# Kernel optimization log

Hardware: AMD Instinct MI355X
Metric: run time of the kernel (lower is better)

The kernel has to match this reference:

```python
import jax, jax.numpy as jnp
import numpy as np

N_NODES = 100000
N_EDGES = 1600000
D = 128
HID = 256  # min(2*D, 256)
D_OUT = 128
BN_EPS = 1e-5


def setup_inputs() -> dict:
    key = jax.random.key(0)
    ks = jax.random.split(key, 16)
    s = 0.05
    inp = {
        "x": jax.random.normal(ks[0], (N_NODES, D), dtype=jnp.float32),
        "edges": jax.random.randint(ks[1], (2, N_EDGES), 0, N_NODES, dtype=jnp.int32),
        # affine_before_rnn: Linear(D, D)
        "W_aff": jax.random.normal(ks[2], (D, D), dtype=jnp.float32) * s,
        "b_aff": jnp.zeros((D,), dtype=jnp.float32),
        # GRUCell(D, D)
        "W_ih": jax.random.normal(ks[3], (3 * D, D), dtype=jnp.float32) * s,
        "b_ih": jnp.zeros((3 * D,), dtype=jnp.float32),
        "W_hh": jax.random.normal(ks[4], (3 * D, D), dtype=jnp.float32) * s,
        "b_hh": jnp.zeros((3 * D,), dtype=jnp.float32),
        # merge_layer: Linear(2*D, D)
        "W_merge": jax.random.normal(ks[5], (D, 2 * D), dtype=jnp.float32) * s,
        "b_merge": jnp.zeros((D,), dtype=jnp.float32),
        # learnable self-connection weight
        "eps": jnp.asarray(1.0, dtype=jnp.float32),
        # backbone: Linear(D, HID) -> relu -> Linear(HID, D_OUT) -> relu -> BatchNorm1d
        "W1": jax.random.normal(ks[6], (HID, D), dtype=jnp.float32) * s,
        "b1": jnp.zeros((HID,), dtype=jnp.float32),
        "W2": jax.random.normal(ks[7], (D_OUT, HID), dtype=jnp.float32) * s,
        "b2": jnp.zeros((D_OUT,), dtype=jnp.float32),
        "gamma": jnp.ones((D_OUT,), dtype=jnp.float32),
        "beta": jnp.zeros((D_OUT,), dtype=jnp.float32),
    }
    return inp


def reference(x, edges, W_aff, b_aff, W_ih, b_ih, W_hh, b_hh,
              W_merge, b_merge, eps, W1, b1, W2, b2, gamma, beta):
    src, dst = edges[0], edges[1]
    n = x.shape[0]

    # ---- aggregation 1: 'sum' -> scatter-sum of neighbor features ----
    agg_sum = jax.ops.segment_sum(x[src], dst, num_segments=n)  # (N, D)

    # ---- aggregation 2: 'rnn-max' -> affine, scatter-max, GRUCell ----
    xi = x @ W_aff.T + b_aff
    agg_max = jax.ops.segment_max(xi[src], dst, num_segments=n)  # (N, D)
    agg_max = jnp.where(jnp.isfinite(agg_max), agg_max, 0.0)  # empty segments -> 0

    # GRUCell: input = aggregated neighbors, hidden = original node features
    gi = agg_max @ W_ih.T + b_ih  # (N, 3D)
    gh = x @ W_hh.T + b_hh        # (N, 3D)
    ir, iz, inn = jnp.split(gi, 3, axis=1)
    hr, hz, hn = jnp.split(gh, 3, axis=1)
    r = jax.nn.sigmoid(ir + hr)
    z = jax.nn.sigmoid(iz + hz)
    ncand = jnp.tanh(inn + r * hn)
    rnn_out = (1.0 - z) * ncand + z * x  # (N, D)

    # ---- merge ('cat') ----
    h = jnp.concatenate([agg_sum, rnn_out], axis=1) @ W_merge.T + b_merge  # (N, D)

    # ---- learnable self-connection ----
    h = h + eps * x

    # ---- backbone: dense -> relu -> dense -> relu -> batchnorm1d (train mode) ----
    h = jax.nn.relu(h @ W1.T + b1)
    h = jax.nn.relu(h @ W2.T + b2)
    mean = jnp.mean(h, axis=0)
    var = jnp.mean(jnp.square(h - mean), axis=0)  # biased batch variance
    out = gamma * (h - mean) * jax.lax.rsqrt(var + BN_EPS) + beta
    return out
```

## Files before the change

### kernel.cpp

```cpp
#include <hip/hip_runtime.h>
#include <hip/hip_bf16.h>
#include <math.h>

using bf16 = __hip_bfloat16;
typedef __attribute__((ext_vector_type(8))) short bf16x8;
typedef __attribute__((ext_vector_type(4))) float f32x4;

__device__ __forceinline__ float b2f(unsigned short u) {
  return __uint_as_float(((unsigned)u) << 16);
}
__device__ __forceinline__ unsigned short f2b(float f) {
  bf16 h = __float2bfloat16(f);
  return *reinterpret_cast<unsigned short*>(&h);
}
__device__ __forceinline__ ushort4 f2b4(float4 v) {
  return make_ushort4(f2b(v.x), f2b(v.y), f2b(v.z), f2b(v.w));
}

__global__ __launch_bounds__(256) void mgemm_k(
    const unsigned short* __restrict__ A, int lda, const float* __restrict__ W,
    const float* __restrict__ bias, unsigned short* __restrict__ Cb, int ldc,
    int N, int M, int K) {
  constexpr int LDA = 72;
  __shared__ unsigned short As[128 * LDA];
  __shared__ unsigned short Ws[128 * LDA];

  const int tid = threadIdx.x;
  const int lane = tid & 63;
  const int wave = tid >> 6;
  const int row0 = blockIdx.y * 128;
  const int m0 = blockIdx.x * 128;
  const int rowhalf = (wave & 1) * 64;
  const int colhalf = (wave >> 1) * 64;
  const int l15 = lane & 15;
  const int quad = lane >> 4;

  f32x4 acc[4][4] = {};

  for (int kc = 0; kc < K; kc += 64) {
#pragma unroll
    for (int i = 0; i < 4; i++) {
      int idx = tid + i * 256;
      int r = idx >> 3;
      int k8 = (idx & 7) * 8;
      int row = row0 + r;
      ushort4 u0 = make_ushort4(0, 0, 0, 0), u1 = u0;
      if (row < N) {
        const unsigned short* s = A + (size_t)row * lda + kc + k8;
        u0 = *(const ushort4*)s;
        u1 = *(const ushort4*)(s + 4);
      }
      *(ushort4*)&As[r * LDA + k8] = u0;
      *(ushort4*)&As[r * LDA + k8 + 4] = u1;
    }
#pragma unroll
    for (int i = 0; i < 8; i++) {
      int idx = tid + i * 256;
      int r = idx >> 4;
      int k4 = idx & 15;
      float4 v = *(const float4*)(W + (size_t)(m0 + r) * K + kc + k4 * 4);
      *(ushort4*)&Ws[r * LDA + k4 * 4] = f2b4(v);
    }
    __syncthreads();
#pragma unroll
    for (int ks = 0; ks < 2; ks++) {
      const int ko = ks * 32 + quad * 8;
      bf16x8 af[4], wf[4];
#pragma unroll
      for (int ri = 0; ri < 4; ri++)
        af[ri] = *(const bf16x8*)&As[(rowhalf + ri * 16 + l15) * LDA + ko];
#pragma unroll
      for (int ci = 0; ci < 4; ci++)
        wf[ci] = *(const bf16x8*)&Ws[(colhalf + ci * 16 + l15) * LDA + ko];
#pragma unroll
      for (int ri = 0; ri < 4; ri++)
#pragma unroll
        for (int ci = 0; ci < 4; ci++)
          acc[ri][ci] = __builtin_amdgcn_mfma_f32_16x16x32_bf16(
              af[ri], wf[ci], acc[ri][ci], 0, 0, 0);
    }
    __syncthreads();
  }
#pragma unroll
  for (int ci = 0; ci < 4; ci++) {
    const int col = m0 + colhalf + ci * 16 + l15;
    const float bv = bias[col];
#pragma unroll
    for (int ri = 0; ri < 4; ri++) {
      const int rbase = row0 + rowhalf + ri * 16 + quad * 4;
#pragma unroll
      for (int r = 0; r < 4; r++) {
        int row = rbase + r;
        if (row >= N) continue;
        Cb[(size_t)row * ldc + col] = f2b(acc[ri][ci][r] + bv);
      }
    }
  }
}

__global__ __launch_bounds__(256) void grubb_k(
    const unsigned short* __restrict__ aggm,
    const unsigned short* __restrict__ xcat,
    const unsigned short* __restrict__ aggs,
    const unsigned short* __restrict__ Wbig,
    const float* __restrict__ bias_big,
    const unsigned short* __restrict__ Wmb, const float* __restrict__ bm,
    const unsigned short* __restrict__ W1b, const float* __restrict__ b1,
    const unsigned short* __restrict__ W2b, const float* __restrict__ b2,
    const float* __restrict__ epsp, float* __restrict__ out,
    float* __restrict__ stats, int N) {
  constexpr int LDA = 264;
  constexpr int LDH = 136;
  __shared__ unsigned short As[32 * LDA];
  __shared__ unsigned short Acat[32 * LDA];
  __shared__ unsigned short Hp[32 * LDH];
  __shared__ float sbn[128], qbn[128];
  unsigned short* Hd = As;

  const int tid = threadIdx.x;
  const int lane = tid & 63;
  const int wave = tid >> 6;
  const int l15 = lane & 15;
  const int quad = lane >> 4;
  const int row0 = blockIdx.x * 32;
  if (tid < 128) {
    sbn[tid] = 0.f;
    qbn[tid] = 0.f;
  }
  const float ep = epsp[0];

  {
    int r = tid >> 3;
    int k32 = (tid & 7) * 32;
    int row = row0 + r;
    uint4 u[4] = {};
    uint4 v[2] = {};
    if (row < N) {
      const unsigned short* s = (k32 < 128)
                                    ? aggm + (size_t)row * 128 + k32
                                    : xcat + (size_t)row * 256 + (k32 - 128);
#pragma unroll
      for (int i = 0; i < 4; i++) u[i] = *(const uint4*)(s + i * 8);
      const unsigned short* s2 = aggs + (size_t)row * 128 + (tid & 7) * 16;
      v[0] = *(const uint4*)s2;
      v[1] = *(const uint4*)(s2 + 8);
    }
#pragma unroll
    for (int i = 0; i < 4; i++) *(uint4*)&As[r * LDA + k32 + i * 8] = u[i];
    int k16 = (tid & 7) * 16;
    *(uint4*)&Acat[r * LDA + k16] = v[0];
    *(uint4*)&Acat[r * LDA + k16 + 8] = v[1];
  }
  __syncthreads();

  {
    f32x4 acc[2][8] = {};
#pragma unroll
    for (int ks = 0; ks < 8; ks++) {
      const int ko = ks * 32 + quad * 8;
      bf16x8 af0 = *(const bf16x8*)&As[l15 * LDA + ko];
      bf16x8 af1 = *(const bf16x8*)&As[(16 + l15) * LDA + ko];
#pragma unroll
      for (int ci = 0; ci < 8; ci++) {
        int m = wave * 128 + ci * 16 + l15;
        bf16x8 wf = *(const bf16x8*)&Wbig[(size_t)m * 256 + ko];
        acc[0][ci] = __builtin_amdgcn_mfma_f32_16x16x32_bf16(af0, wf,
                                                             acc[0][ci], 0, 0, 0);
        acc[1][ci] = __builtin_amdgcn_mfma_f32_16x16x32_bf16(af1, wf,
                                                             acc[1][ci], 0, 0, 0);
      }
    }
#pragma unroll
    for (int fi = 0; fi < 2; fi++) {
      const int f = wave * 32 + fi * 16 + l15;
      const float br = bias_big[f];
      const float bz = bias_big[128 + f];
      const float bi = bias_big[256 + f];
      const float bh = bias_big[384 + f];
#pragma unroll
      for (int ri = 0; ri < 2; ri++) {
#pragma unroll
        for (int r = 0; r < 4; r++) {
          int rl = ri * 16 + quad * 4 + r;
          float rg = 1.f / (1.f + __expf(-(acc[ri][4 * fi + 0][r] + br)));
          float zg = 1.f / (1.f + __expf(-(acc[ri][4 * fi + 1][r] + bz)));
          float a =
              acc[ri][4 * fi + 2][r] + bi + rg * (acc[ri][4 * fi + 3][r] + bh);
          float t = 1.f - 2.f / (__expf(2.f * fabsf(a)) + 1.f);
          float nc = copysignf(t, a);
          float xv = b2f(As[rl * LDA + 128 + f]);
          Acat[rl * LDA + 128 + f] = f2b((1.f - zg) * nc + zg * xv);
        }
      }
    }
  }
  __syncthreads();

  {
    f32x4 accm[2][2] = {};
#pragma unroll
    for (int ks = 0; ks < 8; ks++) {
      const int ko = ks * 32 + quad * 8;
      bf16x8 af[2];
#pragma unroll
      for (int ri = 0; ri < 2; ri++)
        af[ri] = *(const bf16x8*)&Acat[(ri * 16 + l15) * LDA + ko];
#pragma unroll
      for (int ci = 0; ci < 2; ci++) {
        bf16x8 wf =
            *(const bf16x8*)&Wmb[(size_t)(wave * 32 + ci * 16 + l15) * 256 + ko];
#pragma unroll
        for (int ri = 0; ri < 2; ri++)
          accm[ri][ci] = __builtin_amdgcn_mfma_f32_16x16x32_bf16(
              af[ri], wf, accm[ri][ci], 0, 0, 0);
      }
    }
#pragma unroll
    for (int ci = 0; ci < 2; ci++) {
      int c = wave * 32 + ci * 16 + l15;
      float bv = bm[c];
#pragma unroll
      for (int ri = 0; ri < 2; ri++) {
#pragma unroll
        for (int r = 0; r < 4; r++) {
          int rl = ri * 16 + quad * 4 + r;
          float v = accm[ri][ci][r] + bv + ep * b2f(As[rl * LDA + 128 + c]);
          Hp[rl * LDH + c] = f2b(v);
        }
      }
    }
  }
  __syncthreads();

  f32x4 acc3[2][2] = {};
#pragma unroll
  for (int hh = 0; hh < 2; hh++) {
    f32x4 acc2[2][2] = {};
#pragma unroll
    for (int ks = 0; ks < 4; ks++) {
      const int ko = ks * 32 + quad * 8;
      bf16x8 af[2];
#pragma unroll
      for (int ri = 0; ri < 2; ri++)
        af[ri] = *(const bf16x8*)&Hp[(ri * 16 + l15) * LDH + ko];
#pragma unroll
      for (int ci = 0; ci < 2; ci++) {
        bf16x8 wf = *(const bf16x8*)&W1b[(size_t)(hh * 128 + wave * 32 +
                                                  ci * 16 + l15) *
                                             128 +
                                         ko];
#pragma unroll
        for (int ri = 0; ri < 2; ri++)
          acc2[ri][ci] = __builtin_amdgcn_mfma_f32_16x16x32_bf16(
              af[ri], wf, acc2[ri][ci], 0, 0, 0);
      }
    }
    __syncthreads();
#pragma unroll
    for (int ci = 0; ci < 2; ci++) {
      int c = wave * 32 + ci * 16 + l15;
      float bv = b1[hh * 128 + c];
#pragma unroll
      for (int ri = 0; ri < 2; ri++) {
#pragma unroll
        for (int r = 0; r < 4; r++) {
          int rl = ri * 16 + quad * 4 + r;
          Hd[rl * LDH + c] = f2b(fmaxf(acc2[ri][ci][r] + bv, 0.f));
        }
      }
    }
    __syncthreads();
#pragma unroll
    for (int ks = 0; ks < 4; ks++) {
      const int ko = ks * 32 + quad * 8;
      bf16x8 af[2];
#pragma unroll
      for (int ri = 0; ri < 2; ri++)
        af[ri] = *(const bf16x8*)&Hd[(ri * 16 + l15) * LDH + ko];
#pragma unroll
      for (int ci = 0; ci < 2; ci++) {
        bf16x8 wf = *(const bf16x8*)&W2b[(size_t)(wave * 32 + ci * 16 + l15) *
                                             256 +
                                         hh * 128 + ko];
#pragma unroll
        for (int ri = 0; ri < 2; ri++)
          acc3[ri][ci] = __builtin_amdgcn_mfma_f32_16x16x32_bf16(
              af[ri], wf, acc3[ri][ci], 0, 0, 0);
      }
    }
  }
#pragma unroll
  for (int ci = 0; ci < 2; ci++) {
    int c = wave * 32 + ci * 16 + l15;
    float bv = b2[c];
    float s = 0.f, q = 0.f;
#pragma unroll
    for (int ri = 0; ri < 2; ri++) {
#pragma unroll
      for (int r = 0; r < 4; r++) {
        int rl = ri * 16 + quad * 4 + r;
        int row = row0 + rl;
        if (row >= N) continue;
        float v = fmaxf(acc3[ri][ci][r] + bv, 0.f);
        out[(size_t)row * 128 + c] = v;
        s += v;
        q += v * v;
      }
    }
    atomicAdd(&sbn[c], s);
    atomicAdd(&qbn[c], q);
  }
  __syncthreads();
  if (tid < 128) {
    atomicAdd(&stats[tid], sbn[tid]);
    atomicAdd(&stats[128 + tid], qbn[tid]);
  }
}

__global__ __launch_bounds__(256) void prep_k(
    const float* __restrict__ W_ih, const float* __restrict__ b_ih,
    const float* __restrict__ W_hh, const float* __restrict__ b_hh,
    const float* __restrict__ Wm, const float* __restrict__ W1,
    const float* __restrict__ W2, unsigned short* __restrict__ Wbig,
    unsigned short* __restrict__ Wmb, unsigned short* __restrict__ W1b,
    unsigned short* __restrict__ W2b, float* __restrict__ bias_big,
    float* __restrict__ stats, int* __restrict__ deg, int N) {
  int idx = blockIdx.x * 256 + threadIdx.x;
  if (idx < N) deg[idx] = 0;
  if (idx < 32768) {
    int mp = idx >> 6;
    int k4 = (idx & 63) * 4;
    int w = mp >> 7, ci = (mp >> 4) & 7, l15 = mp & 15;
    int g = ci & 3, fi = ci >> 2;
    int f = w * 32 + fi * 16 + l15;
    const float* src = nullptr;
    int koff = 0;
    if (g <= 1) {
      int m = g * 128 + f;
      if (k4 < 128) { src = W_ih + (size_t)m * 128; koff = k4; }
      else          { src = W_hh + (size_t)m * 128; koff = k4 - 128; }
    } else if (g == 2) {
      if (k4 < 128) { src = W_ih + (size_t)(256 + f) * 128; koff = k4; }
    } else {
      if (k4 >= 128) { src = W_hh + (size_t)(256 + f) * 128; koff = k4 - 128; }
    }
    ushort4 o = make_ushort4(0, 0, 0, 0);
    if (src) o = f2b4(*(const float4*)(src + koff));
    *(ushort4*)&Wbig[(size_t)mp * 256 + k4] = o;
  }
  if (idx < 8192) {
    int m = idx >> 6;
    int k4 = (idx & 63) * 4;
    *(ushort4*)&Wmb[(size_t)m * 256 + k4] =
        f2b4(*(const float4*)(Wm + (size_t)m * 256 + k4));
    *(ushort4*)&W2b[(size_t)m * 256 + k4] =
        f2b4(*(const float4*)(W2 + (size_t)m * 256 + k4));
    int m2 = idx >> 5;
    int k42 = (idx & 31) * 4;
    *(ushort4*)&W1b[(size_t)m2 * 128 + k42] =
        f2b4(*(const float4*)(W1 + (size_t)m2 * 128 + k42));
  }
  if (blockIdx.x == 0) {
    int t = threadIdx.x;
    stats[t] = 0.f;
#pragma unroll
    for (int h = 0; h < 2; h++) {
      int mm = t + h * 256;
      float b;
      if (mm < 256) b = b_ih[mm] + b_hh[mm];
      else if (mm < 384) b = b_ih[mm];
      else b = b_hh[mm - 128];
      bias_big[mm] = b;
    }
  }
}

__global__ __launch_bounds__(256) void cvthist_k(
    const int* __restrict__ edges, int* __restrict__ deg, int E,
    const float* __restrict__ x, unsigned short* __restrict__ xcat,
    int ngroups, int eblk) {
  if ((int)blockIdx.x < eblk) {
    int e = blockIdx.x * 256 + threadIdx.x;
    if (e < E) atomicAdd(&deg[edges[(size_t)E + e]], 1);
  } else {
    int g = (blockIdx.x - eblk) * 256 + threadIdx.x;
    if (g >= ngroups) return;
    int n = g >> 5;
    int j = (g & 31) * 4;
    float4 v = *(const float4*)&x[(size_t)n * 128 + j];
    *(ushort4*)&xcat[(size_t)n * 256 + j] = f2b4(v);
  }
}

__global__ __launch_bounds__(256) void scan1_k(const int* __restrict__ deg,
                                               int* __restrict__ off,
                                               int* __restrict__ bsums, int N) {
  __shared__ int s[256];
  int t = threadIdx.x;
  int i = blockIdx.x * 256 + t;
  int v = (i < N) ? deg[i] : 0;
  s[t] = v;
  __syncthreads();
#pragma unroll
  for (int d = 1; d < 256; d <<= 1) {
    int u = (t >= d) ? s[t - d] : 0;
    __syncthreads();
    s[t] += u;
    __syncthreads();
  }
  if (i < N) off[i] = s[t] - v;
  if (t == 255) bsums[blockIdx.x] = s[255];
}

__global__ __launch_bounds__(512) void scan2_k(int* __restrict__ bsums,
                                               int nb) {
  __shared__ int s[512];
  int t = threadIdx.x;
  int v = (t < nb) ? bsums[t] : 0;
  s[t] = v;
  __syncthreads();
#pragma unroll
  for (int d = 1; d < 512; d <<= 1) {
    int u = (t >= d) ? s[t - d] : 0;
    __syncthreads();
    s[t] += u;
    __syncthreads();
  }
  if (t < nb) bsums[t] = s[t] - v;
}

__global__ __launch_bounds__(256) void scan3_k(int* __restrict__ off,
                                               const int* __restrict__ bsums,
                                               int* __restrict__ binoff,
                                               int* __restrict__ bincur,
                                               int N, int E, int NB) {
  int i = blockIdx.x * 256 + threadIdx.x;
  if (i < N) {
    int o = off[i] + bsums[blockIdx.x];
    off[i] = o;
    if ((i & 511) == 0) {
      binoff[i >> 9] = o;
      bincur[i >> 9] = o;
    }
  }
  if (i == 0) {
    off[N] = E;
    binoff[NB] = E;
  }
}

__global__ __launch_bounds__(256) void edgepart_k(const int* __restrict__ edges,
                                                  int* __restrict__ bincur,
                                                  int* __restrict__ part,
                                                  int E, int NB) {
  __shared__ int cnt[256];
  const int tid = threadIdx.x;
  if (tid < NB) cnt[tid] = 0;
  __syncthreads();
  int sv[16], dv[16];
  const int e0 = blockIdx.x * 4096;
#pragma unroll
  for (int i = 0; i < 16; i++) {
    int e = e0 + i * 256 + tid;
    int s = 0, d = -1;
    if (e < E) {
      s = edges[e];
      d = edges[(size_t)E + e];
    }
    sv[i] = s;
    dv[i] = d;
    if (d >= 0) atomicAdd(&cnt[d >> 9], 1);
  }
  __syncthreads();
  if (tid < NB) {
    int c = cnt[tid];
    int base = c ? atomicAdd(&bincur[tid], c) : 0;
    cnt[tid] = base;
  }
  __syncthreads();
#pragma unroll
  for (int i = 0; i < 16; i++) {
    int d = dv[i];
    if (d < 0) continue;
    int p = atomicAdd(&cnt[d >> 9], 1);
    part[p] = (sv[i] << 9) | (d & 511);
  }
}

__global__ __launch_bounds__(1024) void fill2_k(const int* __restrict__ off,
                                                const int* __restrict__ binoff,
                                                const int* __restrict__ part,
                                                int* __restrict__ bucket,
                                                int N) {
  __shared__ int scur[512];
  const int b = blockIdx.x;
  const int n0 = b << 9;
  const int tid = threadIdx.x;
  if (tid < 512) {
    int node = n0 + tid;
    scur[tid] = (node < N) ? off[node] : 0;
  }
  __syncthreads();
  const int j0 = binoff[b];
  const int j1 = binoff[b + 1];
  for (int j = j0 + tid; j < j1; j += 1024) {
    int p = part[j];
    int pos = atomicAdd(&scur[p & 511], 1);
    bucket[pos] = p >> 9;
  }
}

__global__ __launch_bounds__(256) void gather_k(
    const int* __restrict__ off, const int* __restrict__ bucket,
    const unsigned short* __restrict__ xcat, unsigned short* __restrict__ aggm,
    unsigned short* __restrict__ aggs, int N) {
  int node = blockIdx.x * 4 + (threadIdx.x >> 6);
  if (node >= N) return;
  const int lane = threadIdx.x & 63;
  const int half = lane >> 5;
  const int f = (lane & 31) * 4;
  const int j0 = off[node], jend = off[node + 1];
  float s0 = 0.f, s1 = 0.f, s2 = 0.f, s3 = 0.f;
  float m0 = -INFINITY, m1 = -INFINITY, m2 = -INFINITY, m3 = -INFINITY;
  int jj = j0 + half;
  int p0 = (jj < jend) ? bucket[jj] : 0;
  int p1 = (jj + 2 < jend) ? bucket[jj + 2] : 0;
  for (; jj < jend; jj += 2) {
    int src = p0;
    p0 = p1;
    p1 = (jj + 4 < jend) ? bucket[jj + 4] : 0;
    ushort4 a = *(const ushort4*)(xcat + (size_t)src * 256 + f);
    ushort4 b = *(const ushort4*)(xcat + (size_t)src * 256 + 128 + f);
    s0 += b2f(a.x);
    s1 += b2f(a.y);
    s2 += b2f(a.z);
    s3 += b2f(a.w);
    m0 = fmaxf(m0, b2f(b.x));
    m1 = fmaxf(m1, b2f(b.y));
    m2 = fmaxf(m2, b2f(b.z));
    m3 = fmaxf(m3, b2f(b.w));
  }
  s0 += __shfl_xor(s0, 32);
  s1 += __shfl_xor(s1, 32);
  s2 += __shfl_xor(s2, 32);
  s3 += __shfl_xor(s3, 32);
  m0 = fmaxf(m0, __shfl_xor(m0, 32));
  m1 = fmaxf(m1, __shfl_xor(m1, 32));
  m2 = fmaxf(m2, __shfl_xor(m2, 32));
  m3 = fmaxf(m3, __shfl_xor(m3, 32));
  if (half == 0) {
    bool nz = jend > j0;
    ushort4 mv = nz ? make_ushort4(f2b(m0), f2b(m1), f2b(m2), f2b(m3))
                    : make_ushort4(0, 0, 0, 0);
    *(ushort4*)&aggm[(size_t)node * 128 + f] = mv;
    *(ushort4*)&aggs[(size_t)node * 128 + f] =
        make_ushort4(f2b(s0), f2b(s1), f2b(s2), f2b(s3));
  }
}

__global__ __launch_bounds__(256) void bn_apply_k(
    float* __restrict__ out, const float* __restrict__ stats,
    const float* __restrict__ gamma, const float* __restrict__ beta,
    float invn, int nd4) {
  int g = blockIdx.x * 256 + threadIdx.x;
  if (g >= nd4) return;
  int d = (g & 31) * 4;
  float4 v = ((float4*)out)[g];
  float o[4] = {v.x, v.y, v.z, v.w};
#pragma unroll
  for (int i = 0; i < 4; i++) {
    float mean = stats[d + i] * invn;
    float var = fmaxf(stats[128 + d + i] * invn - mean * mean, 0.f);
    float sc = gamma[d + i] * rsqrtf(var + 1e-5f);
    o[i] = (o[i] - mean) * sc + beta[d + i];
  }
  ((float4*)out)[g] = make_float4(o[0], o[1], o[2], o[3]);
}

extern "C" void kernel_launch(void* const* d_in, const int* in_sizes, int n_in,
                              void* d_out, int out_size, void* d_ws,
                              size_t ws_size, hipStream_t stream) {
  (void)n_in;
  (void)out_size;
  (void)ws_size;
  const float* x = (const float*)d_in[0];
  const int* edges = (const int*)d_in[1];
  const float* W_aff = (const float*)d_in[2];
  const float* b_aff = (const float*)d_in[3];
  const float* W_ih = (const float*)d_in[4];
  const float* b_ih = (const float*)d_in[5];
  const float* W_hh = (const float*)d_in[6];
  const float* b_hh = (const float*)d_in[7];
  const float* W_merge = (const float*)d_in[8];
  const float* b_merge = (const float*)d_in[9];
  const float* epsp = (const float*)d_in[10];
  const float* W1 = (const float*)d_in[11];
  const float* b1 = (const float*)d_in[12];
  const float* W2 = (const float*)d_in[13];
  const float* b2 = (const float*)d_in[14];
  const float* gamma = (const float*)d_in[15];
  const float* beta = (const float*)d_in[16];

  const int N = in_sizes[0] / 128;
  const int E = in_sizes[1] / 2;
  const size_t nd = (size_t)N * 128;
  const int NB = (N + 511) >> 9;

  char* base = (char*)d_ws;
  unsigned short* xcat = (unsigned short*)base;
  unsigned short* aggs = (unsigned short*)(base + (size_t)N * 512);
  unsigned short* aggm = (unsigned short*)(base + (size_t)N * 1024);
  unsigned short* Wbig = (unsigned short*)(base + (size_t)N * 1280);
  unsigned short* Wmb = Wbig + 512 * 256;
  unsigned short* W1b = Wmb + 128 * 256;
  unsigned short* W2b = W1b + 256 * 128;
  float* bias_big = (float*)(W2b + 128 * 256);
  float* stats = bias_big + 512;
  int* deg = (int*)(stats + 512);
  int* off = deg + N;
  int* binoff = off + N + 1;
  int* bincur = binoff + NB + 1;
  int* bucket = bincur + NB;
  int* bsums = bucket + E;
  float* out = (float*)d_out;
  int* part = (int*)d_out;

  const int ny = (N + 127) / 128;
  const int nblk = (N + 255) / 256;
  const int eblk = (E + 255) / 256;
  const int cvtblk = (int)((nd / 4 + 255) / 256);
  const int pgrid = nblk > 128 ? nblk : 128;
  dim3 blk(256);

  prep_k<<<pgrid, blk, 0, stream>>>(W_ih, b_ih, W_hh, b_hh, W_merge, W1, W2,
                                    Wbig, Wmb, W1b, W2b, bias_big, stats, deg,
                                    N);
  cvthist_k<<<eblk + cvtblk, blk, 0, stream>>>(edges, deg, E, x, xcat,
                                               (int)(nd / 4), eblk);
  scan1_k<<<nblk, blk, 0, stream>>>(deg, off, bsums, N);
  scan2_k<<<1, 512, 0, stream>>>(bsums, nblk);
  scan3_k<<<nblk, blk, 0, stream>>>(off, bsums, binoff, bincur, N, E, NB);
  edgepart_k<<<(E + 4095) / 4096, blk, 0, stream>>>(edges, bincur, part, E, NB);
  fill2_k<<<NB, dim3(1024), 0, stream>>>(off, binoff, part, bucket, N);

  mgemm_k<<<dim3(1, ny), blk, 0, stream>>>(xcat, 256, W_aff, b_aff, xcat + 128,
                                           256, N, 128, 128);
  gather_k<<<(N + 3) / 4, blk, 0, stream>>>(off, bucket, xcat, aggm, aggs, N);
  grubb_k<<<(N + 31) / 32, blk, 0, stream>>>(aggm, xcat, aggs, Wbig, bias_big,
                                             Wmb, b_merge, W1b, b1, W2b, b2,
                                             epsp, out, stats, N);
  bn_apply_k<<<(int)((nd / 4 + 255) / 256), blk, 0, stream>>>(
      out, stats, gamma, beta, 1.f / (float)N, (int)(nd / 4));
}
```

Baseline: 620.4 us.

## Software-prefetch weight fragments and alias Hp onto Acat to raise occupancy

Weight fragments for the GRU, merge, and both backbone GEMMs in the fused kernel are now double-buffered in registers, so global loads for the next k-step are issued before the current MFMAs run. The Hp LDS buffer is removed and aliased onto Acat, with an extra barrier after the merge GEMM, to cut shared memory per block. launch_bounds now requests 4 blocks per CU. The extra prefetch registers plus the occupancy hint could cause spills or stricter register limits.

```diff
diff --git a/kernel.cpp b/kernel.cpp
--- a/kernel.cpp
+++ b/kernel.cpp
@@ -98,7 +98,7 @@
   }
 }
 
-__global__ __launch_bounds__(256) void grubb_k(
+__global__ __launch_bounds__(256, 4) void grubb_k(
     const unsigned short* __restrict__ aggm,
     const unsigned short* __restrict__ xcat,
     const unsigned short* __restrict__ aggs,
@@ -113,9 +113,9 @@
   constexpr int LDH = 136;
   __shared__ unsigned short As[32 * LDA];
   __shared__ unsigned short Acat[32 * LDA];
-  __shared__ unsigned short Hp[32 * LDH];
   __shared__ float sbn[128], qbn[128];
   unsigned short* Hd = As;
+  unsigned short* Hp = Acat;
 
   const int tid = threadIdx.x;
   const int lane = tid & 63;
@@ -154,20 +154,39 @@
   __syncthreads();
 
   {
+    const unsigned short* wptr =
+        Wbig + (size_t)(wave * 128 + l15) * 256 + quad * 8;
     f32x4 acc[2][8] = {};
+    bf16x8 wfA[4], wfB[4];
+#pragma unroll
+    for (int ci = 0; ci < 4; ci++)
+      wfA[ci] = *(const bf16x8*)(wptr + ci * 16 * 256);
 #pragma unroll
     for (int ks = 0; ks < 8; ks++) {
       const int ko = ks * 32 + quad * 8;
       bf16x8 af0 = *(const bf16x8*)&As[l15 * LDA + ko];
       bf16x8 af1 = *(const bf16x8*)&As[(16 + l15) * LDA + ko];
 #pragma unroll
-      for (int ci = 0; ci < 8; ci++) {
-        int m = wave * 128 + ci * 16 + l15;
-        bf16x8 wf = *(const bf16x8*)&Wbig[(size_t)m * 256 + ko];
-        acc[0][ci] = __builtin_amdgcn_mfma_f32_16x16x32_bf16(af0, wf,
+      for (int ci = 0; ci < 4; ci++)
+        wfB[ci] = *(const bf16x8*)(wptr + (ci + 4) * 16 * 256 + ks * 32);
+#pragma unroll
+      for (int ci = 0; ci < 4; ci++) {
+        acc[0][ci] = __builtin_amdgcn_mfma_f32_16x16x32_bf16(af0, wfA[ci],
                                                              acc[0][ci], 0, 0, 0);
-        acc[1][ci] = __builtin_amdgcn_mfma_f32_16x16x32_bf16(af1, wf,
+        acc[1][ci] = __builtin_amdgcn_mfma_f32_16x16x32_bf16(af1, wfA[ci],
                                                              acc[1][ci], 0, 0, 0);
+      }
+      if (ks < 7) {
+#pragma unroll
+        for (int ci = 0; ci < 4; ci++)
+          wfA[ci] = *(const bf16x8*)(wptr + ci * 16 * 256 + (ks + 1) * 32);
+      }
+#pragma unroll
+      for (int ci = 0; ci < 4; ci++) {
+        acc[0][4 + ci] = __builtin_amdgcn_mfma_f32_16x16x32_bf16(
+            af0, wfB[ci], acc[0][4 + ci], 0, 0, 0);
+        acc[1][4 + ci] = __builtin_amdgcn_mfma_f32_16x16x32_bf16(
+            af1, wfB[ci], acc[1][4 + ci], 0, 0, 0);
       }
     }
 #pragma unroll
@@ -196,8 +215,12 @@
   }
   __syncthreads();
 
+  f32x4 accm[2][2] = {};
   {
-    f32x4 accm[2][2] = {};
+    const unsigned short* wptr =
+        Wmb + (size_t)(wave * 32 + l15) * 256 + quad * 8;
+    bf16x8 w0 = *(const bf16x8*)(wptr);
+    bf16x8 w1 = *(const bf16x8*)(wptr + 16 * 256);
 #pragma unroll
     for (int ks = 0; ks < 8; ks++) {
       const int ko = ks * 32 + quad * 8;
@@ -205,16 +228,26 @@
 #pragma unroll
       for (int ri = 0; ri < 2; ri++)
         af[ri] = *(const bf16x8*)&Acat[(ri * 16 + l15) * LDA + ko];
-#pragma unroll
-      for (int ci = 0; ci < 2; ci++) {
-        bf16x8 wf =
-            *(const bf16x8*)&Wmb[(size_t)(wave * 32 + ci * 16 + l15) * 256 + ko];
-#pragma unroll
-        for (int ri = 0; ri < 2; ri++)
-          accm[ri][ci] = __builtin_amdgcn_mfma_f32_16x16x32_bf16(
-              af[ri], wf, accm[ri][ci], 0, 0, 0);
-      }
-    }
+      bf16x8 n0, n1;
+      if (ks < 7) {
+        n0 = *(const bf16x8*)(wptr + (ks + 1) * 32);
+        n1 = *(const bf16x8*)(wptr + 16 * 256 + (ks + 1) * 32);
+      }
+#pragma unroll
+      for (int ri = 0; ri < 2; ri++) {
+        accm[ri][0] = __builtin_amdgcn_mfma_f32_16x16x32_bf16(af[ri], w0,
+                                                              accm[ri][0], 0, 0, 0);
+        accm[ri][1] = __builtin_amdgcn_mfma_f32_16x16x32_bf16(af[ri], w1,
+                                                              accm[ri][1], 0, 0, 0);
+      }
+      if (ks < 7) {
+        w0 = n0;
+        w1 = n1;
+      }
+    }
+  }
+  __syncthreads();
+  {
 #pragma unroll
     for (int ci = 0; ci < 2; ci++) {
       int c = wave * 32 + ci * 16 + l15;
@@ -236,23 +269,34 @@
 #pragma unroll
   for (int hh = 0; hh < 2; hh++) {
     f32x4 acc2[2][2] = {};
-#pragma unroll
-    for (int ks = 0; ks < 4; ks++) {
-      const int ko = ks * 32 + quad * 8;
-      bf16x8 af[2];
-#pragma unroll
-      for (int ri = 0; ri < 2; ri++)
-        af[ri] = *(const bf16x8*)&Hp[(ri * 16 + l15) * LDH + ko];
-#pragma unroll
-      for (int ci = 0; ci < 2; ci++) {
-        bf16x8 wf = *(const bf16x8*)&W1b[(size_t)(hh * 128 + wave * 32 +
-                                                  ci * 16 + l15) *
-                                             128 +
-                                         ko];
+    {
+      const unsigned short* wptr =
+          W1b + (size_t)(hh * 128 + wave * 32 + l15) * 128 + quad * 8;
+      bf16x8 w0 = *(const bf16x8*)(wptr);
+      bf16x8 w1 = *(const bf16x8*)(wptr + 16 * 128);
+#pragma unroll
+      for (int ks = 0; ks < 4; ks++) {
+        const int ko = ks * 32 + quad * 8;
+        bf16x8 af[2];
 #pragma unroll
         for (int ri = 0; ri < 2; ri++)
-          acc2[ri][ci] = __builtin_amdgcn_mfma_f32_16x16x32_bf16(
-              af[ri], wf, acc2[ri][ci], 0, 0, 0);
+          af[ri] = *(const bf16x8*)&Hp[(ri * 16 + l15) * LDH + ko];
+        bf16x8 n0, n1;
+        if (ks < 3) {
+          n0 = *(const bf16x8*)(wptr + (ks + 1) * 32);
+          n1 = *(const bf16x8*)(wptr + 16 * 128 + (ks + 1) * 32);
+        }
+#pragma unroll
+        for (int ri = 0; ri < 2; ri++) {
+          acc2[ri][0] = __builtin_amdgcn_mfma_f32_16x16x32_bf16(
+              af[ri], w0, acc2[ri][0], 0, 0, 0);
+          acc2[ri][1] = __builtin_amdgcn_mfma_f32_16x16x32_bf16(
+              af[ri], w1, acc2[ri][1], 0, 0, 0);
+        }
+        if (ks < 3) {
+          w0 = n0;
+          w1 = n1;
+        }
       }
     }
     __syncthreads();
@@ -270,22 +314,34 @@
       }
     }
     __syncthreads();
-#pragma unroll
-    for (int ks = 0; ks < 4; ks++) {
-      const int ko = ks * 32 + quad * 8;
-      bf16x8 af[2];
-#pragma unroll
-      for (int ri = 0; ri < 2; ri++)
-        af[ri] = *(const bf16x8*)&Hd[(ri * 16 + l15) * LDH + ko];
-#pragma unroll
-      for (int ci = 0; ci < 2; ci++) {
-        bf16x8 wf = *(const bf16x8*)&W2b[(size_t)(wave * 32 + ci * 16 + l15) *
-                                             256 +
-                                         hh * 128 + ko];
+    {
+      const unsigned short* wptr =
+          W2b + (size_t)(wave * 32 + l15) * 256 + hh * 128 + quad * 8;
+      bf16x8 w0 = *(const bf16x8*)(wptr);
+      bf16x8 w1 = *(const bf16x8*)(wptr + 16 * 256);
+#pragma unroll
+      for (int ks = 0; ks < 4; ks++) {
+        const int ko = ks * 32 + quad * 8;
+        bf16x8 af[2];
 #pragma unroll
         for (int ri = 0; ri < 2; ri++)
-          acc3[ri][ci] = __builtin_amdgcn_mfma_f32_16x16x32_bf16(
-              af[ri], wf, acc3[ri][ci], 0, 0, 0);
+          af[ri] = *(const bf16x8*)&Hd[(ri * 16 + l15) * LDH + ko];
+        bf16x8 n0, n1;
+        if (ks < 3) {
+          n0 = *(const bf16x8*)(wptr + (ks + 1) * 32);
+          n1 = *(const bf16x8*)(wptr + 16 * 256 + (ks + 1) * 32);
+        }
+#pragma unroll
+        for (int ri = 0; ri < 2; ri++) {
+          acc3[ri][0] = __builtin_amdgcn_mfma_f32_16x16x32_bf16(
+              af[ri], w0, acc3[ri][0], 0, 0, 0);
+          acc3[ri][1] = __builtin_amdgcn_mfma_f32_16x16x32_bf16(
+              af[ri], w1, acc3[ri][1], 0, 0, 0);
+        }
+        if (ks < 3) {
+          w0 = n0;
+          w1 = n1;
+        }
       }
     }
   }
```

After: 630.8 us. About the same (+1.7%).
